# Performance work log

Measured on AMD Instinct MI355X. Metric: run time of the kernel, lower is better.

Reference implementation:

```python
import jax, jax.numpy as jnp
import numpy as np

HIDDEN = 2048
HEADS = 16
HEAD_DIM = HIDDEN // HEADS
BATCH = 2
SEQ = 2048


def setup_inputs() -> dict:
    key = jax.random.key(0)
    ks = jax.random.split(key, 9)
    s = 0.02
    return {
        "x": jax.random.normal(ks[0], (BATCH, SEQ, HIDDEN), dtype=jnp.float32),
        "wq": jax.random.normal(ks[1], (HIDDEN, HIDDEN), dtype=jnp.float32) * s,
        "bq": jax.random.normal(ks[2], (HIDDEN,), dtype=jnp.float32) * s,
        "wk": jax.random.normal(ks[3], (HIDDEN, HIDDEN), dtype=jnp.float32) * s,
        "bk": jax.random.normal(ks[4], (HIDDEN,), dtype=jnp.float32) * s,
        "wv": jax.random.normal(ks[5], (HIDDEN, HIDDEN), dtype=jnp.float32) * s,
        "bv": jax.random.normal(ks[6], (HIDDEN,), dtype=jnp.float32) * s,
        "wo": jax.random.normal(ks[7], (HIDDEN, HIDDEN), dtype=jnp.float32) * s,
        "bo": jax.random.normal(ks[8], (HIDDEN,), dtype=jnp.float32) * s,
    }


def reference(x, wq, bq, wk, bk, wv, bv, wo, bo):
    B, S, _ = x.shape
    scale = jnp.sqrt(jnp.float32(HEAD_DIM))
    # torch Linear: y = x @ W.T + b
    def proj(w, b):
        return (x @ w.T + b).reshape(B, S, HEADS, HEAD_DIM).transpose(0, 2, 1, 3)
    q = proj(wq, bq)  # [B,H,S,D]
    k = proj(wk, bk)
    v = proj(wv, bv)
    scores = jnp.einsum("bhqd,bhkd->bhqk", q, k) / scale  # [B,H,S,S]
    probs = jax.nn.softmax(scores, axis=-1)
    ctx = jnp.einsum("bhqk,bhkd->bhqd", probs, v)  # [B,H,S,D]
    ctx = ctx.transpose(0, 2, 1, 3).reshape(B, S, HIDDEN)
    return ctx @ wo.T + bo
```

## Files before the change

kernel.cpp:

```cpp
#include <hip/hip_runtime.h>

typedef unsigned short u16;
typedef unsigned int   u32;
typedef float  f32x4   __attribute__((ext_vector_type(4)));
typedef __bf16 bf16x8  __attribute__((ext_vector_type(8)));
typedef u16    u16x8   __attribute__((ext_vector_type(8)));
typedef u16    u16x4   __attribute__((ext_vector_type(4)));
typedef u32    u32x2   __attribute__((ext_vector_type(2)));
typedef u32    u32x4   __attribute__((ext_vector_type(4)));

#define HIDDEN 2048
#define SEQ    2048
#define NHEADS 16
#define HD     128
#define BATCH  2
#define QSTR   4096

typedef const __attribute__((address_space(3))) u16* lptr;

__device__ __forceinline__ u16 f2bf(float f) {
  u32 u = __builtin_bit_cast(u32, f);
  u += 0x7FFFu + ((u >> 16) & 1u);
  return (u16)(u >> 16);
}
__device__ __forceinline__ u32 pk2(float a, float b) {
  __bf16 x = (__bf16)a, y = (__bf16)b;
  return (u32)__builtin_bit_cast(u16, x) | ((u32)__builtin_bit_cast(u16, y) << 16);
}
__device__ __forceinline__ bf16x8 ld_frag(const u16* p) {
  return __builtin_bit_cast(bf16x8, *(const u32x4*)p);
}
__device__ __forceinline__ void gload_lds16(const u16* g, u16* l) {
  __builtin_amdgcn_global_load_lds((const __attribute__((address_space(1))) u32*)g,
                                   (__attribute__((address_space(3))) u32*)l, 16, 0, 0);
}

#define DSR(dst, base, lit) \
  asm volatile("ds_read_b128 %0, %1 offset:" lit : "=v"(dst) : "v"(base))

__global__ __launch_bounds__(256) void cvt_kernel(const float* __restrict__ src,
                                                  u16* __restrict__ dst, int n4) {
  int stride = gridDim.x * blockDim.x;
  for (int i = blockIdx.x * blockDim.x + threadIdx.x; i < n4; i += stride) {
    f32x4 v = ((const f32x4*)src)[i];
    u16x4 o;
    o[0] = f2bf(v[0]); o[1] = f2bf(v[1]); o[2] = f2bf(v[2]); o[3] = f2bf(v[3]);
    *(u16x4*)(dst + (size_t)i * 4) = o;
  }
}

__global__ __launch_bounds__(256) void cvt4_kernel(
    const float* __restrict__ s0, const float* __restrict__ s1,
    const float* __restrict__ s2, const float* __restrict__ s3,
    u16* __restrict__ o0, u16* __restrict__ o1,
    u16* __restrict__ o2, u16* __restrict__ o3, int n4) {
  const float* src = (blockIdx.y == 0) ? s0 : (blockIdx.y == 1) ? s1 : (blockIdx.y == 2) ? s2 : s3;
  u16* dst = (blockIdx.y == 0) ? o0 : (blockIdx.y == 1) ? o1 : (blockIdx.y == 2) ? o2 : o3;
  int stride = gridDim.x * blockDim.x;
  for (int i = blockIdx.x * blockDim.x + threadIdx.x; i < n4; i += stride) {
    f32x4 v = ((const f32x4*)src)[i];
    u16x4 o;
    o[0] = f2bf(v[0]); o[1] = f2bf(v[1]); o[2] = f2bf(v[2]); o[3] = f2bf(v[3]);
    *(u16x4*)(dst + (size_t)i * 4) = o;
  }
}

__global__ __launch_bounds__(512, 2) void gemm_qkv(
    const u16* __restrict__ A, const u16* __restrict__ Bt,
    const float* __restrict__ bq, const float* __restrict__ bk,
    const float* __restrict__ bv,
    u16* __restrict__ qk, u16* __restrict__ vtb, float qscale)
{
  __shared__ __attribute__((aligned(16))) u16 As[2][16384];
  __shared__ __attribute__((aligned(16))) u16 Bs[2][12288];

  const int tid  = threadIdx.x;
  const int lane = tid & 63;
  const int wave = tid >> 6;
  const int l15  = lane & 15;
  const int g    = lane >> 4;
  const int wm   = wave >> 2;
  const int wn   = wave & 3;

  const int id  = blockIdx.x;
  const int xcd = id & 7;
  const int c   = id >> 3;
  const int tileN = (xcd * 4 + (c >> 4)) * 192;
  const int tileM = (c & 15) << 8;

  const int srow = tid >> 3;
  const int gch8 = ((tid & 7) ^ (srow & 7)) * 8;
  const u16* agp = A  + (size_t)(tileM + srow) * HIDDEN + gch8;
  const u16* bgp = Bt + (size_t)(tileN + srow) * HIDDEN + gch8;
  u16* asp = (u16*)&As[0][0] + tid * 8;
  u16* bsp = (u16*)&Bs[0][0] + tid * 8;

  auto stage = [&](int buf, int ko) {
    u16* ad = asp + buf * 16384;
    u16* bd = bsp + buf * 12288;
#pragma unroll
    for (int r = 0; r < 4; ++r)
      gload_lds16(agp + (size_t)r * 64 * HIDDEN + ko, ad + r * 4096);
#pragma unroll
    for (int r = 0; r < 3; ++r)
      gload_lds16(bgp + (size_t)r * 64 * HIDDEN + ko, bd + r * 4096);
  };

  const int sw = l15 & 7;
  const int c0 = (g ^ sw) * 8;
  const int c1 = ((g ^ sw) ^ 4) * 8;
  lptr aT = (lptr)&As[0][0] + (size_t)(wm * 128 + l15) * 64;
  lptr bT = (lptr)&Bs[0][0] + (size_t)(wn * 48 + l15) * 64;

  f32x4 acc[8][3] = {};
  bf16x8 Xa[8], Xb[3], Ya[8], Yb[3];

#define ISSUE_SET(Sa, Sb, ab, bb)      \
  DSR(Sa[0], ab, "0");                 \
  DSR(Sa[1], ab, "2048");              \
  DSR(Sa[2], ab, "4096");              \
  DSR(Sa[3], ab, "6144");              \
  DSR(Sa[4], ab, "8192");              \
  DSR(Sa[5], ab, "10240");             \
  DSR(Sa[6], ab, "12288");             \
  DSR(Sa[7], ab, "14336");             \
  DSR(Sb[0], bb, "0");                 \
  DSR(Sb[1], bb, "2048");              \
  DSR(Sb[2], bb, "4096");

#define MFMA24(Sa, Sb)                                                                    \
  _Pragma("unroll")                                                                       \
  for (int mf = 0; mf < 8; ++mf) {                                                        \
    _Pragma("unroll")                                                                     \
    for (int nf = 0; nf < 3; ++nf)                                                        \
      acc[mf][nf] = __builtin_amdgcn_mfma_f32_16x16x32_bf16(Sa[mf], Sb[nf], acc[mf][nf], 0, 0, 0); \
  }

  stage(0, 0);
  stage(1, 64);
  asm volatile("s_waitcnt vmcnt(7)" ::: "memory");
  __builtin_amdgcn_s_barrier();
  __builtin_amdgcn_sched_barrier(0);
  {
    lptr ab = aT + c0;
    lptr bb = bT + c0;
    ISSUE_SET(Xa, Xb, ab, bb)
  }

#pragma unroll 2
  for (int t = 0; t < 32; ++t) {
    const int cur = t & 1;
    lptr aC = aT + cur * 16384;
    lptr bC = bT + cur * 12288;
    {
      lptr ab = aC + c1;
      lptr bb = bC + c1;
      ISSUE_SET(Ya, Yb, ab, bb)
    }
    asm volatile("s_waitcnt lgkmcnt(11)" ::: "memory");
    __builtin_amdgcn_sched_barrier(0);
    __builtin_amdgcn_s_setprio(1);
    MFMA24(Xa, Xb)
    __builtin_amdgcn_s_setprio(0);
    asm volatile("s_waitcnt lgkmcnt(0)" ::: "memory");
    __builtin_amdgcn_sched_barrier(0);
    __builtin_amdgcn_s_setprio(1);
    MFMA24(Ya, Yb)
    __builtin_amdgcn_s_setprio(0);
    __builtin_amdgcn_s_barrier();
    __builtin_amdgcn_sched_barrier(0);
    if (t < 30) {
      stage(cur, (t + 2) * 64);
      asm volatile("s_waitcnt vmcnt(7)" ::: "memory");
    } else {
      asm volatile("s_waitcnt vmcnt(0)" ::: "memory");
    }
    __builtin_amdgcn_s_barrier();
    __builtin_amdgcn_sched_barrier(0);
    if (t < 31) {
      lptr ab = aT + (cur ^ 1) * 16384 + c0;
      lptr bb = bT + (cur ^ 1) * 12288 + c0;
      ISSUE_SET(Xa, Xb, ab, bb)
    }
  }

#pragma unroll
  for (int mi = 0; mi < 8; ++mi) {
#pragma unroll
    for (int ni = 0; ni < 3; ++ni) {
      const int gcb = tileN + wn * 48 + ni * 16;
      const int seg = gcb >> 11;
      const int gc  = gcb + l15;
      const float bvv = ((seg == 0) ? bq : (seg == 1) ? bk : bv)[gc & 2047];
      if (seg < 2) {
        const float scl = (seg == 0) ? qscale : 1.f;
#pragma unroll
        for (int j = 0; j < 4; ++j) {
          const int gr = tileM + wm * 128 + mi * 16 + g * 4 + j;
          qk[(size_t)gr * QSTR + gc] = f2bf((acc[mi][ni][j] + bvv) * scl);
        }
      } else {
        const int dglob = gc - 4096;
        const int hh = dglob >> 7, dd = dglob & 127;
        const int srow0 = tileM + wm * 128 + mi * 16 + g * 4;
        const int bb = srow0 >> 11, ss = srow0 & 2047;
        u16x4 o;
#pragma unroll
        for (int j = 0; j < 4; ++j) o[j] = f2bf(acc[mi][ni][j] + bvv);
        *(u16x4*)(vtb + ((size_t)((bb * NHEADS + hh) * HD + dd)) * SEQ + ss) = o;
      }
    }
  }
#undef ISSUE_SET
#undef MFMA24
}

__global__ __launch_bounds__(256, 2) void gemm_bt(
    const u16* __restrict__ A, const u16* __restrict__ Bt,
    const float* __restrict__ bias, float* __restrict__ Cout,
    int M, int N, int K)
{
  __shared__ __attribute__((aligned(16))) u16 As[128 * 32];
  __shared__ __attribute__((aligned(16))) u16 Bs[128 * 32];
  const int tid  = threadIdx.x;
  const int lane = tid & 63;
  const int wave = tid >> 6;

  const int nbx   = N >> 7;
  const int nby   = M >> 7;
  const int id    = blockIdx.x;
  const int xcd   = id & 7;
  const int c     = id >> 3;
  const int cpx   = nbx >> 3;
  const int tileN = (xcd * cpx + c / nby) << 7;
  const int tileM = (c % nby) << 7;

  const int g = lane >> 4, r = lane & 15;

  const int srow = lane >> 2;
  const int scol = (lane & 3) * 8;
  const u16* ag0 = A  + (size_t)(tileM + wave * 16 + srow) * K + scol;
  const u16* ag1 = ag0 + (size_t)64 * K;
  const u16* bg0 = Bt + (size_t)(tileN + wave * 16 + srow) * K + scol;
  const u16* bg1 = bg0 + (size_t)64 * K;
  u16* as0 = &As[wave * 512];
  u16* as1 = &As[(wave + 4) * 512];
  u16* bs0 = &Bs[wave * 512];
  u16* bs1 = &Bs[(wave + 4) * 512];

  const int wm = wave >> 1, wn = wave & 1;
  const u16* afp = &As[(wm * 64 + r) * 32 + g * 8];
  const u16* bfp = &Bs[(wn * 64 + r) * 32 + g * 8];

  f32x4 acc[4][4] = {};

  for (int kt = 0; kt < K; kt += 32) {
    __syncthreads();
    gload_lds16(ag0 + kt, as0);
    gload_lds16(ag1 + kt, as1);
    gload_lds16(bg0 + kt, bs0);
    gload_lds16(bg1 + kt, bs1);
    __syncthreads();
    bf16x8 af[4], bf[4];
#pragma unroll
    for (int mi = 0; mi < 4; mi++) af[mi] = ld_frag(afp + mi * 512);
#pragma unroll
    for (int ni = 0; ni < 4; ni++) bf[ni] = ld_frag(bfp + ni * 512);
#pragma unroll
    for (int mi = 0; mi < 4; mi++)
#pragma unroll
      for (int ni = 0; ni < 4; ni++)
        acc[mi][ni] = __builtin_amdgcn_mfma_f32_16x16x32_bf16(af[mi], bf[ni], acc[mi][ni], 0, 0, 0);
  }

#pragma unroll
  for (int mi = 0; mi < 4; mi++) {
#pragma unroll
    for (int ni = 0; ni < 4; ni++) {
      const int gc = tileN + wn * 64 + ni * 16 + r;
      const float bv = bias[gc];
#pragma unroll
      for (int j = 0; j < 4; j++) {
        const int gr = tileM + wm * 64 + mi * 16 + g * 4 + j;
        Cout[(size_t)gr * N + gc] = acc[mi][ni][j] + bv;
      }
    }
  }
}

__global__ __launch_bounds__(256, 2) void attn_kernel(
    const u16* __restrict__ QKg, const u16* __restrict__ Vtg, u16* __restrict__ Ctx)
{
  __shared__ __attribute__((aligned(16))) u16 Ks[2][32 * 128];
  __shared__ __attribute__((aligned(16))) u16 Vs[2][128 * 32];

  const int tid  = threadIdx.x;
  const int lane = tid & 63;
  const int wave = tid >> 6;
  const int g4   = lane >> 4;
  const int l15  = lane & 15;

  const int wg = ((blockIdx.x & 7) << 6) + (blockIdx.x >> 3);
  const int bh = wg >> 4;
  const int qt = wg & 15;
  const int b  = bh >> 4, h = bh & 15;

  const u16* Qb  = QKg + (size_t)b * SEQ * QSTR + (size_t)h * HD;
  const u16* Kb  = Qb + 2048;
  const u16* Vth = Vtg + (size_t)bh * HD * SEQ;
  u16* Cb = Ctx + (size_t)b * SEQ * HIDDEN + (size_t)h * HD;

  const int qbase = qt * 128 + wave * 32 + l15;

  bf16x8 qf[2][4];
#pragma unroll
  for (int qs = 0; qs < 2; qs++)
#pragma unroll
    for (int dc = 0; dc < 4; dc++)
      qf[qs][dc] = ld_frag(Qb + (size_t)(qbase + qs * 16) * QSTR + dc * 32 + g4 * 8);

  const int kvp0 = (l15 >> 2) * 8 + (l15 & 3);
  const int msw  = (l15 & 3) | (((l15 >> 2) & 1) << 2);

  f32x4 ctx[2][8] = {};
  float m_run[2] = {-1e30f, -1e30f};
  float l_run[2] = {0.f, 0.f};

  auto stage = [&](int buf, int kv0) {
#pragma unroll
    for (int i = 0; i < 2; i++) {
      const int idx = tid + i * 256;
      const int kv = idx >> 4, up = idx & 15;
      const int um = up ^ ((kv & 3) | (((kv >> 3) & 1) << 2));
      gload_lds16(Kb + (size_t)(kv0 + kv) * QSTR + um * 8, &Ks[buf][idx * 8]);
      const int d = idx >> 2, u = idx & 3;
      gload_lds16(Vth + (size_t)d * SEQ + kv0 + u * 8, &Vs[buf][idx * 8]);
    }
  };

  stage(0, 0);
  __syncthreads();

  const int NT = SEQ / 32;
  for (int t = 0; t < NT; t++) {
    const int buf = t & 1;
    if (t + 1 < NT) stage(buf ^ 1, (t + 1) * 32);

    f32x4 s[2][2] = {};
    __builtin_amdgcn_s_setprio(1);
#pragma unroll
    for (int ni = 0; ni < 2; ni++) {
      const int row = kvp0 + ni * 4;
#pragma unroll
      for (int dc = 0; dc < 4; dc++) {
        bf16x8 kf = ld_frag(&Ks[buf][row * 128 + (((dc * 4 + g4) ^ msw) * 8)]);
        s[0][ni] = __builtin_amdgcn_mfma_f32_16x16x32_bf16(kf, qf[0][dc], s[0][ni], 0, 0, 0);
        s[1][ni] = __builtin_amdgcn_mfma_f32_16x16x32_bf16(kf, qf[1][dc], s[1][ni], 0, 0, 0);
      }
    }
    __builtin_amdgcn_s_setprio(0);

    bool ok0, ok1;
    float pmax[2];
#pragma unroll
    for (int qs = 0; qs < 2; qs++) {
      pmax[qs] = fmaxf(fmaxf(fmaxf(s[qs][0][0], s[qs][0][1]), fmaxf(s[qs][0][2], s[qs][0][3])),
                       fmaxf(fmaxf(s[qs][1][0], s[qs][1][1]), fmaxf(s[qs][1][2], s[qs][1][3])));
      pmax[qs] = fmaxf(pmax[qs], __shfl_xor(pmax[qs], 16));
      pmax[qs] = fmaxf(pmax[qs], __shfl_xor(pmax[qs], 32));
    }
    ok0 = (pmax[0] <= m_run[0] + 8.f);
    ok1 = (pmax[1] <= m_run[1] + 8.f);
    if (!__all(ok0 && ok1)) {
#pragma unroll
      for (int qs = 0; qs < 2; qs++) {
        const float mn = fmaxf(m_run[qs], pmax[qs]);
        const float corr = exp2f(m_run[qs] - mn);
        m_run[qs] = mn;
        l_run[qs] *= corr;
#pragma unroll
        for (int dt = 0; dt < 8; dt++)
#pragma unroll
          for (int j = 0; j < 4; j++) ctx[qs][dt][j] *= corr;
      }
    }
    bf16x8 pfrag[2];
#pragma unroll
    for (int qs = 0; qs < 2; qs++) {
      float ps = 0.f;
#pragma unroll
      for (int ni = 0; ni < 2; ni++)
#pragma unroll
        for (int j = 0; j < 4; j++) {
          const float p = exp2f(s[qs][ni][j] - m_run[qs]);
          s[qs][ni][j] = p;
          ps += p;
        }
      ps += __shfl_xor(ps, 16);
      ps += __shfl_xor(ps, 32);
      l_run[qs] += ps;
      u32x4 pw;
      pw[0] = pk2(s[qs][0][0], s[qs][0][1]);
      pw[1] = pk2(s[qs][0][2], s[qs][0][3]);
      pw[2] = pk2(s[qs][1][0], s[qs][1][1]);
      pw[3] = pk2(s[qs][1][2], s[qs][1][3]);
      pfrag[qs] = __builtin_bit_cast(bf16x8, pw);
    }

    __builtin_amdgcn_s_setprio(1);
#pragma unroll
    for (int dt = 0; dt < 8; dt++) {
      bf16x8 vf = ld_frag(&Vs[buf][(dt * 16 + l15) * 32 + g4 * 8]);
      ctx[0][dt] = __builtin_amdgcn_mfma_f32_16x16x32_bf16(vf, pfrag[0], ctx[0][dt], 0, 0, 0);
      ctx[1][dt] = __builtin_amdgcn_mfma_f32_16x16x32_bf16(vf, pfrag[1], ctx[1][dt], 0, 0, 0);
    }
    __builtin_amdgcn_s_setprio(0);

    __syncthreads();
  }

#pragma unroll
  for (int qs = 0; qs < 2; qs++) {
    const float linv = 1.f / l_run[qs];
    u16* crow = Cb + (size_t)(qbase + qs * 16) * HIDDEN;
#pragma unroll
    for (int dt = 0; dt < 8; dt++) {
      u16x4 o;
#pragma unroll
      for (int j = 0; j < 4; j++) o[j] = f2bf(ctx[qs][dt][j] * linv);
      *(u16x4*)&crow[dt * 16 + g4 * 4] = o;
    }
  }
}

extern "C" void kernel_launch(void* const* d_in, const int* in_sizes, int n_in,
                              void* d_out, int out_size, void* d_ws, size_t ws_size,
                              hipStream_t stream) {
  (void)in_sizes; (void)n_in; (void)out_size; (void)ws_size;
  const float* x  = (const float*)d_in[0];
  const float* wq = (const float*)d_in[1];
  const float* bq = (const float*)d_in[2];
  const float* wk = (const float*)d_in[3];
  const float* bk = (const float*)d_in[4];
  const float* wv = (const float*)d_in[5];
  const float* bv = (const float*)d_in[6];
  const float* wo = (const float*)d_in[7];
  const float* bo = (const float*)d_in[8];

  const size_t NX = (size_t)BATCH * SEQ * HIDDEN;
  const size_t NW = (size_t)HIDDEN * HIDDEN;
  u16* xb   = (u16*)d_ws;
  u16* wqb  = xb  + NX;
  u16* wkb  = wqb + NW;
  u16* wvb  = wkb + NW;
  u16* wob  = wvb + NW;
  u16* qk   = wob + NW;
  u16* vtb  = qk  + 2 * NX;
  u16* ctxb = xb;

  cvt_kernel<<<2048, 256, 0, stream>>>(x, xb, (int)(NX / 4));
  cvt4_kernel<<<dim3(512, 4), 256, 0, stream>>>(wq, wk, wv, wo, wqb, wkb, wvb, wob, (int)(NW / 4));

  const float qscale = 0.12751744174240807f;
  gemm_qkv<<<512, 512, 0, stream>>>(xb, wqb, bq, bk, bv, qk, vtb, qscale);

  attn_kernel<<<512, 256, 0, stream>>>(qk, vtb, ctxb);

  gemm_bt<<<512, 256, 0, stream>>>(ctxb, wob, bo, (float*)d_out, BATCH * SEQ, HIDDEN, HIDDEN);
}
```

Before: 289.6 us.

## Halve attention query tile per wave and double grid with V LDS swizzle

Each wave now handles 16 query rows instead of 32, so a workgroup covers 64 queries, the grid doubles to 1024 blocks and launch bounds allow 4 blocks per CU. This frees registers and raises occupancy so more waves can hide latency on the 256 CUs. In exchange every K/V tile is loaded and staged twice as often per query, because each staged tile now feeds half as many queries. An XOR swizzle is also added to the V staging and reads to cut LDS bank conflicts.

```diff
diff --git a/kernel.cpp b/kernel.cpp
--- a/kernel.cpp
+++ b/kernel.cpp
@@ -288,7 +288,7 @@
   }
 }
 
-__global__ __launch_bounds__(256, 2) void attn_kernel(
+__global__ __launch_bounds__(256, 4) void attn_kernel(
     const u16* __restrict__ QKg, const u16* __restrict__ Vtg, u16* __restrict__ Ctx)
 {
   __shared__ __attribute__((aligned(16))) u16 Ks[2][32 * 128];
@@ -300,9 +300,9 @@
   const int g4   = lane >> 4;
   const int l15  = lane & 15;
 
-  const int wg = ((blockIdx.x & 7) << 6) + (blockIdx.x >> 3);
-  const int bh = wg >> 4;
-  const int qt = wg & 15;
+  const int wg = ((blockIdx.x & 7) << 7) + (blockIdx.x >> 3);
+  const int bh = wg >> 5;
+  const int qt = wg & 31;
   const int b  = bh >> 4, h = bh & 15;
 
   const u16* Qb  = QKg + (size_t)b * SEQ * QSTR + (size_t)h * HD;
@@ -310,21 +310,20 @@
   const u16* Vth = Vtg + (size_t)bh * HD * SEQ;
   u16* Cb = Ctx + (size_t)b * SEQ * HIDDEN + (size_t)h * HD;
 
-  const int qbase = qt * 128 + wave * 32 + l15;
-
-  bf16x8 qf[2][4];
-#pragma unroll
-  for (int qs = 0; qs < 2; qs++)
-#pragma unroll
-    for (int dc = 0; dc < 4; dc++)
-      qf[qs][dc] = ld_frag(Qb + (size_t)(qbase + qs * 16) * QSTR + dc * 32 + g4 * 8);
+  const int qbase = qt * 64 + wave * 16 + l15;
+
+  bf16x8 qf[4];
+#pragma unroll
+  for (int dc = 0; dc < 4; dc++)
+    qf[dc] = ld_frag(Qb + (size_t)qbase * QSTR + dc * 32 + g4 * 8);
 
   const int kvp0 = (l15 >> 2) * 8 + (l15 & 3);
   const int msw  = (l15 & 3) | (((l15 >> 2) & 1) << 2);
-
-  f32x4 ctx[2][8] = {};
-  float m_run[2] = {-1e30f, -1e30f};
-  float l_run[2] = {0.f, 0.f};
+  const int vch  = (g4 ^ (l15 >> 2)) * 8;
+
+  f32x4 ctx[8] = {};
+  float m_run = -1e30f;
+  float l_run = 0.f;
 
   auto stage = [&](int buf, int kv0) {
 #pragma unroll
@@ -334,7 +333,8 @@
       const int um = up ^ ((kv & 3) | (((kv >> 3) & 1) << 2));
       gload_lds16(Kb + (size_t)(kv0 + kv) * QSTR + um * 8, &Ks[buf][idx * 8]);
       const int d = idx >> 2, u = idx & 3;
-      gload_lds16(Vth + (size_t)d * SEQ + kv0 + u * 8, &Vs[buf][idx * 8]);
+      const int uv = u ^ ((d >> 2) & 3);
+      gload_lds16(Vth + (size_t)d * SEQ + kv0 + uv * 8, &Vs[buf][idx * 8]);
     }
   };
 
@@ -346,7 +346,7 @@
     const int buf = t & 1;
     if (t + 1 < NT) stage(buf ^ 1, (t + 1) * 32);
 
-    f32x4 s[2][2] = {};
+    f32x4 s[2] = {};
     __builtin_amdgcn_s_setprio(1);
 #pragma unroll
     for (int ni = 0; ni < 2; ni++) {
@@ -354,82 +354,63 @@
 #pragma unroll
       for (int dc = 0; dc < 4; dc++) {
         bf16x8 kf = ld_frag(&Ks[buf][row * 128 + (((dc * 4 + g4) ^ msw) * 8)]);
-        s[0][ni] = __builtin_amdgcn_mfma_f32_16x16x32_bf16(kf, qf[0][dc], s[0][ni], 0, 0, 0);
-        s[1][ni] = __builtin_amdgcn_mfma_f32_16x16x32_bf16(kf, qf[1][dc], s[1][ni], 0, 0, 0);
+        s[ni] = __builtin_amdgcn_mfma_f32_16x16x32_bf16(kf, qf[dc], s[ni], 0, 0, 0);
       }
     }
     __builtin_amdgcn_s_setprio(0);
 
-    bool ok0, ok1;
-    float pmax[2];
-#pragma unroll
-    for (int qs = 0; qs < 2; qs++) {
-      pmax[qs] = fmaxf(fmaxf(fmaxf(s[qs][0][0], s[qs][0][1]), fmaxf(s[qs][0][2], s[qs][0][3])),
-                       fmaxf(fmaxf(s[qs][1][0], s[qs][1][1]), fmaxf(s[qs][1][2], s[qs][1][3])));
-      pmax[qs] = fmaxf(pmax[qs], __shfl_xor(pmax[qs], 16));
-      pmax[qs] = fmaxf(pmax[qs], __shfl_xor(pmax[qs], 32));
-    }
-    ok0 = (pmax[0] <= m_run[0] + 8.f);
-    ok1 = (pmax[1] <= m_run[1] + 8.f);
-    if (!__all(ok0 && ok1)) {
-#pragma unroll
-      for (int qs = 0; qs < 2; qs++) {
-        const float mn = fmaxf(m_run[qs], pmax[qs]);
-        const float corr = exp2f(m_run[qs] - mn);
-        m_run[qs] = mn;
-        l_run[qs] *= corr;
-#pragma unroll
-        for (int dt = 0; dt < 8; dt++)
-#pragma unroll
-          for (int j = 0; j < 4; j++) ctx[qs][dt][j] *= corr;
+    float pmax = fmaxf(fmaxf(fmaxf(s[0][0], s[0][1]), fmaxf(s[0][2], s[0][3])),
+                       fmaxf(fmaxf(s[1][0], s[1][1]), fmaxf(s[1][2], s[1][3])));
+    pmax = fmaxf(pmax, __shfl_xor(pmax, 16));
+    pmax = fmaxf(pmax, __shfl_xor(pmax, 32));
+    if (!__all(pmax <= m_run + 8.f)) {
+      const float mn = fmaxf(m_run, pmax);
+      const float corr = exp2f(m_run - mn);
+      m_run = mn;
+      l_run *= corr;
+#pragma unroll
+      for (int dt = 0; dt < 8; dt++)
+#pragma unroll
+        for (int j = 0; j < 4; j++) ctx[dt][j] *= corr;
+    }
+    float ps = 0.f;
+#pragma unroll
+    for (int ni = 0; ni < 2; ni++)
+#pragma unroll
+      for (int j = 0; j < 4; j++) {
+        const float p = exp2f(s[ni][j] - m_run);
+        s[ni][j] = p;
+        ps += p;
       }
-    }
-    bf16x8 pfrag[2];
-#pragma unroll
-    for (int qs = 0; qs < 2; qs++) {
-      float ps = 0.f;
-#pragma unroll
-      for (int ni = 0; ni < 2; ni++)
-#pragma unroll
-        for (int j = 0; j < 4; j++) {
-          const float p = exp2f(s[qs][ni][j] - m_run[qs]);
-          s[qs][ni][j] = p;
-          ps += p;
-        }
-      ps += __shfl_xor(ps, 16);
-      ps += __shfl_xor(ps, 32);
-      l_run[qs] += ps;
-      u32x4 pw;
-      pw[0] = pk2(s[qs][0][0], s[qs][0][1]);
-      pw[1] = pk2(s[qs][0][2], s[qs][0][3]);
-      pw[2] = pk2(s[qs][1][0], s[qs][1][1]);
-      pw[3] = pk2(s[qs][1][2], s[qs][1][3]);
-      pfrag[qs] = __builtin_bit_cast(bf16x8, pw);
-    }
+    ps += __shfl_xor(ps, 16);
+    ps += __shfl_xor(ps, 32);
+    l_run += ps;
+    u32x4 pw;
+    pw[0] = pk2(s[0][0], s[0][1]);
+    pw[1] = pk2(s[0][2], s[0][3]);
+    pw[2] = pk2(s[1][0], s[1][1]);
+    pw[3] = pk2(s[1][2], s[1][3]);
+    const bf16x8 pfrag = __builtin_bit_cast(bf16x8, pw);
 
     __builtin_amdgcn_s_setprio(1);
 #pragma unroll
     for (int dt = 0; dt < 8; dt++) {
-      bf16x8 vf = ld_frag(&Vs[buf][(dt * 16 + l15) * 32 + g4 * 8]);
-      ctx[0][dt] = __builtin_amdgcn_mfma_f32_16x16x32_bf16(vf, pfrag[0], ctx[0][dt], 0, 0, 0);
-      ctx[1][dt] = __builtin_amdgcn_mfma_f32_16x16x32_bf16(vf, pfrag[1], ctx[1][dt], 0, 0, 0);
+      bf16x8 vf = ld_frag(&Vs[buf][(dt * 16 + l15) * 32 + vch]);
+      ctx[dt] = __builtin_amdgcn_mfma_f32_16x16x32_bf16(vf, pfrag, ctx[dt], 0, 0, 0);
     }
     __builtin_amdgcn_s_setprio(0);
 
     __syncthreads();
   }
 
-#pragma unroll
-  for (int qs = 0; qs < 2; qs++) {
-    const float linv = 1.f / l_run[qs];
-    u16* crow = Cb + (size_t)(qbase + qs * 16) * HIDDEN;
-#pragma unroll
-    for (int dt = 0; dt < 8; dt++) {
-      u16x4 o;
-#pragma unroll
-      for (int j = 0; j < 4; j++) o[j] = f2bf(ctx[qs][dt][j] * linv);
-      *(u16x4*)&crow[dt * 16 + g4 * 4] = o;
-    }
+  const float linv = 1.f / l_run;
+  u16* crow = Cb + (size_t)qbase * HIDDEN;
+#pragma unroll
+  for (int dt = 0; dt < 8; dt++) {
+    u16x4 o;
+#pragma unroll
+    for (int j = 0; j < 4; j++) o[j] = f2bf(ctx[dt][j] * linv);
+    *(u16x4*)&crow[dt * 16 + g4 * 4] = o;
   }
 }
 
@@ -464,7 +445,7 @@
   const float qscale = 0.12751744174240807f;
   gemm_qkv<<<512, 512, 0, stream>>>(xb, wqb, bq, bk, bv, qk, vtb, qscale);
 
-  attn_kernel<<<512, 256, 0, stream>>>(qk, vtb, ctxb);
+  attn_kernel<<<1024, 256, 0, stream>>>(qk, vtb, ctxb);
 
   gemm_bt<<<512, 256, 0, stream>>>(ctxb, wob, bo, (float*)d_out, BATCH * SEQ, HIDDEN, HIDDEN);
 }
```

New measurement: 289.6 us. About the same (-0.0%).

## Widen attention KV tile to 64 with batched LDS reads and explicit waitcnt pipelining

Applied to the files above, without the earlier changes.

The attention kernel now processes 64 keys per iteration instead of 32, doubling the K/V LDS buffers. V gets an XOR-swizzled layout, and staging addresses are precomputed once outside the loop. K and V fragments are fetched up front with inline ds_read_b128, and MFMAs are split around partial lgkmcnt waits under sched_barriers. The full __syncthreads is replaced by explicit vmcnt waits plus s_barrier. The aim is to halve loop and barrier overhead and overlap LDS latency with MFMA work, at the cost of more LDS and registers, which may reduce occupancy.

```diff
diff --git a/kernel.cpp b/kernel.cpp
--- a/kernel.cpp
+++ b/kernel.cpp
@@ -37,6 +37,8 @@
 
 #define DSR(dst, base, lit) \
   asm volatile("ds_read_b128 %0, %1 offset:" lit : "=v"(dst) : "v"(base))
+
+#define MFMA16(d, a, b) d = __builtin_amdgcn_mfma_f32_16x16x32_bf16(a, b, d, 0, 0, 0)
 
 __global__ __launch_bounds__(256) void cvt_kernel(const float* __restrict__ src,
                                                   u16* __restrict__ dst, int n4) {
@@ -291,8 +293,8 @@
 __global__ __launch_bounds__(256, 2) void attn_kernel(
     const u16* __restrict__ QKg, const u16* __restrict__ Vtg, u16* __restrict__ Ctx)
 {
-  __shared__ __attribute__((aligned(16))) u16 Ks[2][32 * 128];
-  __shared__ __attribute__((aligned(16))) u16 Vs[2][128 * 32];
+  __shared__ __attribute__((aligned(16))) u16 Ks[2][64 * 128];
+  __shared__ __attribute__((aligned(16))) u16 Vs[2][128 * 64];
 
   const int tid  = threadIdx.x;
   const int lane = tid & 63;
@@ -321,56 +323,114 @@
 
   const int kvp0 = (l15 >> 2) * 8 + (l15 & 3);
   const int msw  = (l15 & 3) | (((l15 >> 2) & 1) << 2);
+  const int msw3 = msw & 3;
+  const int mk   = (l15 >> 2) & 1;
+  const int kcol = (g4 ^ msw3) * 8;
+
+  lptr ksb = (lptr)&Ks[0][0];
+  lptr kE0 = ksb + (kvp0      ) * 128 + kcol + mk * 32;
+  lptr kO0 = ksb + (kvp0      ) * 128 + kcol + (1 ^ mk) * 32;
+  lptr kE1 = ksb + (kvp0 +   4) * 128 + kcol + mk * 32;
+  lptr kO1 = ksb + (kvp0 +   4) * 128 + kcol + (1 ^ mk) * 32;
+  lptr kE2 = ksb + (kvp0 +  32) * 128 + kcol + mk * 32;
+  lptr kO2 = ksb + (kvp0 +  32) * 128 + kcol + (1 ^ mk) * 32;
+  lptr kE3 = ksb + (kvp0 +  36) * 128 + kcol + mk * 32;
+  lptr kO3 = ksb + (kvp0 +  36) * 128 + kcol + (1 ^ mk) * 32;
+
+  lptr vsb = (lptr)&Vs[0][0];
+  lptr vB0 = vsb + l15 * 64 + ((0 * 4 + g4) ^ (l15 & 7)) * 8;
+  lptr vB1 = vsb + l15 * 64 + ((1 * 4 + g4) ^ (l15 & 7)) * 8;
+
+  const u16* kg[4];
+  const u16* vg[4];
+  u16* ksd = (u16*)&Ks[0][0] + tid * 8;
+  u16* vsd = (u16*)&Vs[0][0] + tid * 8;
+#pragma unroll
+  for (int i = 0; i < 4; i++) {
+    const int idx = tid + i * 256;
+    const int kv = idx >> 4, up = idx & 15;
+    const int um = up ^ ((kv & 3) | (((kv >> 3) & 1) << 2));
+    kg[i] = Kb + (size_t)kv * QSTR + um * 8;
+    const int d = idx >> 3, u = idx & 7;
+    const int uv = u ^ (d & 7);
+    vg[i] = Vth + (size_t)d * SEQ + uv * 8;
+  }
+
+  auto stage = [&](int buf, int kv0) {
+    u16* kd = ksd + buf * 8192;
+    u16* vd = vsd + buf * 8192;
+#pragma unroll
+    for (int i = 0; i < 4; i++) gload_lds16(kg[i] + (size_t)kv0 * QSTR, kd + i * 2048);
+#pragma unroll
+    for (int i = 0; i < 4; i++) gload_lds16(vg[i] + kv0, vd + i * 2048);
+  };
 
   f32x4 ctx[2][8] = {};
   float m_run[2] = {-1e30f, -1e30f};
   float l_run[2] = {0.f, 0.f};
 
-  auto stage = [&](int buf, int kv0) {
-#pragma unroll
-    for (int i = 0; i < 2; i++) {
-      const int idx = tid + i * 256;
-      const int kv = idx >> 4, up = idx & 15;
-      const int um = up ^ ((kv & 3) | (((kv >> 3) & 1) << 2));
-      gload_lds16(Kb + (size_t)(kv0 + kv) * QSTR + um * 8, &Ks[buf][idx * 8]);
-      const int d = idx >> 2, u = idx & 3;
-      gload_lds16(Vth + (size_t)d * SEQ + kv0 + u * 8, &Vs[buf][idx * 8]);
-    }
-  };
-
   stage(0, 0);
-  __syncthreads();
-
-  const int NT = SEQ / 32;
+
+  const int NT = SEQ / 64;
   for (int t = 0; t < NT; t++) {
     const int buf = t & 1;
-    if (t + 1 < NT) stage(buf ^ 1, (t + 1) * 32);
-
-    f32x4 s[2][2] = {};
+
+    if (t + 1 < NT) {
+      stage(buf ^ 1, (t + 1) * 64);
+      asm volatile("s_waitcnt vmcnt(8)" ::: "memory");
+    } else {
+      asm volatile("s_waitcnt vmcnt(0)" ::: "memory");
+    }
+    __builtin_amdgcn_s_barrier();
+    __builtin_amdgcn_sched_barrier(0);
+
+    bf16x8 kf[4][4];
+    {
+      const int bo = buf * 8192;
+      lptr e0 = kE0 + bo, o0 = kO0 + bo, e1 = kE1 + bo, o1 = kO1 + bo;
+      lptr e2 = kE2 + bo, o2 = kO2 + bo, e3 = kE3 + bo, o3 = kO3 + bo;
+      DSR(kf[0][0], e0, "0"); DSR(kf[0][1], o0, "0"); DSR(kf[0][2], e0, "128"); DSR(kf[0][3], o0, "128");
+      DSR(kf[1][0], e1, "0"); DSR(kf[1][1], o1, "0"); DSR(kf[1][2], e1, "128"); DSR(kf[1][3], o1, "128");
+      DSR(kf[2][0], e2, "0"); DSR(kf[2][1], o2, "0"); DSR(kf[2][2], e2, "128"); DSR(kf[2][3], o2, "128");
+      DSR(kf[3][0], e3, "0"); DSR(kf[3][1], o3, "0"); DSR(kf[3][2], e3, "128"); DSR(kf[3][3], o3, "128");
+    }
+    f32x4 s[2][4] = {};
+    asm volatile("s_waitcnt lgkmcnt(8)" ::: "memory");
+    __builtin_amdgcn_sched_barrier(0);
     __builtin_amdgcn_s_setprio(1);
 #pragma unroll
-    for (int ni = 0; ni < 2; ni++) {
-      const int row = kvp0 + ni * 4;
+    for (int ni = 0; ni < 2; ni++)
 #pragma unroll
       for (int dc = 0; dc < 4; dc++) {
-        bf16x8 kf = ld_frag(&Ks[buf][row * 128 + (((dc * 4 + g4) ^ msw) * 8)]);
-        s[0][ni] = __builtin_amdgcn_mfma_f32_16x16x32_bf16(kf, qf[0][dc], s[0][ni], 0, 0, 0);
-        s[1][ni] = __builtin_amdgcn_mfma_f32_16x16x32_bf16(kf, qf[1][dc], s[1][ni], 0, 0, 0);
+        MFMA16(s[0][ni], kf[ni][dc], qf[0][dc]);
+        MFMA16(s[1][ni], kf[ni][dc], qf[1][dc]);
       }
-    }
+    __builtin_amdgcn_sched_barrier(0);
+    asm volatile("s_waitcnt lgkmcnt(0)" ::: "memory");
+    __builtin_amdgcn_sched_barrier(0);
+#pragma unroll
+    for (int ni = 2; ni < 4; ni++)
+#pragma unroll
+      for (int dc = 0; dc < 4; dc++) {
+        MFMA16(s[0][ni], kf[ni][dc], qf[0][dc]);
+        MFMA16(s[1][ni], kf[ni][dc], qf[1][dc]);
+      }
     __builtin_amdgcn_s_setprio(0);
-
-    bool ok0, ok1;
+    __builtin_amdgcn_sched_barrier(0);
+
     float pmax[2];
 #pragma unroll
     for (int qs = 0; qs < 2; qs++) {
-      pmax[qs] = fmaxf(fmaxf(fmaxf(s[qs][0][0], s[qs][0][1]), fmaxf(s[qs][0][2], s[qs][0][3])),
-                       fmaxf(fmaxf(s[qs][1][0], s[qs][1][1]), fmaxf(s[qs][1][2], s[qs][1][3])));
+      float m0 = fmaxf(fmaxf(s[qs][0][0], s[qs][0][1]), fmaxf(s[qs][0][2], s[qs][0][3]));
+      float m1 = fmaxf(fmaxf(s[qs][1][0], s[qs][1][1]), fmaxf(s[qs][1][2], s[qs][1][3]));
+      float m2 = fmaxf(fmaxf(s[qs][2][0], s[qs][2][1]), fmaxf(s[qs][2][2], s[qs][2][3]));
+      float m3 = fmaxf(fmaxf(s[qs][3][0], s[qs][3][1]), fmaxf(s[qs][3][2], s[qs][3][3]));
+      pmax[qs] = fmaxf(fmaxf(m0, m1), fmaxf(m2, m3));
       pmax[qs] = fmaxf(pmax[qs], __shfl_xor(pmax[qs], 16));
       pmax[qs] = fmaxf(pmax[qs], __shfl_xor(pmax[qs], 32));
     }
-    ok0 = (pmax[0] <= m_run[0] + 8.f);
-    ok1 = (pmax[1] <= m_run[1] + 8.f);
+    const bool ok0 = (pmax[0] <= m_run[0] + 8.f);
+    const bool ok1 = (pmax[1] <= m_run[1] + 8.f);
     if (!__all(ok0 && ok1)) {
 #pragma unroll
       for (int qs = 0; qs < 2; qs++) {
@@ -384,12 +444,12 @@
           for (int j = 0; j < 4; j++) ctx[qs][dt][j] *= corr;
       }
     }
-    bf16x8 pfrag[2];
+    bf16x8 pfrag[2][2];
 #pragma unroll
     for (int qs = 0; qs < 2; qs++) {
       float ps = 0.f;
 #pragma unroll
-      for (int ni = 0; ni < 2; ni++)
+      for (int ni = 0; ni < 4; ni++)
 #pragma unroll
         for (int j = 0; j < 4; j++) {
           const float p = exp2f(s[qs][ni][j] - m_run[qs]);
@@ -399,24 +459,52 @@
       ps += __shfl_xor(ps, 16);
       ps += __shfl_xor(ps, 32);
       l_run[qs] += ps;
-      u32x4 pw;
-      pw[0] = pk2(s[qs][0][0], s[qs][0][1]);
-      pw[1] = pk2(s[qs][0][2], s[qs][0][3]);
-      pw[2] = pk2(s[qs][1][0], s[qs][1][1]);
-      pw[3] = pk2(s[qs][1][2], s[qs][1][3]);
-      pfrag[qs] = __builtin_bit_cast(bf16x8, pw);
-    }
-
+#pragma unroll
+      for (int hh = 0; hh < 2; hh++) {
+        u32x4 pw;
+        pw[0] = pk2(s[qs][2 * hh][0], s[qs][2 * hh][1]);
+        pw[1] = pk2(s[qs][2 * hh][2], s[qs][2 * hh][3]);
+        pw[2] = pk2(s[qs][2 * hh + 1][0], s[qs][2 * hh + 1][1]);
+        pw[3] = pk2(s[qs][2 * hh + 1][2], s[qs][2 * hh + 1][3]);
+        pfrag[qs][hh] = __builtin_bit_cast(bf16x8, pw);
+      }
+    }
+    __builtin_amdgcn_sched_barrier(0);
+
+    bf16x8 vf[2][8];
+    {
+      lptr v0 = vB0 + buf * 8192;
+      lptr v1 = vB1 + buf * 8192;
+      DSR(vf[0][0], v0, "0");     DSR(vf[0][1], v0, "2048");
+      DSR(vf[0][2], v0, "4096");  DSR(vf[0][3], v0, "6144");
+      DSR(vf[0][4], v0, "8192");  DSR(vf[0][5], v0, "10240");
+      DSR(vf[0][6], v0, "12288"); DSR(vf[0][7], v0, "14336");
+      DSR(vf[1][0], v1, "0");     DSR(vf[1][1], v1, "2048");
+      DSR(vf[1][2], v1, "4096");  DSR(vf[1][3], v1, "6144");
+      DSR(vf[1][4], v1, "8192");  DSR(vf[1][5], v1, "10240");
+      DSR(vf[1][6], v1, "12288"); DSR(vf[1][7], v1, "14336");
+    }
+    asm volatile("s_waitcnt lgkmcnt(8)" ::: "memory");
+    __builtin_amdgcn_sched_barrier(0);
     __builtin_amdgcn_s_setprio(1);
 #pragma unroll
     for (int dt = 0; dt < 8; dt++) {
-      bf16x8 vf = ld_frag(&Vs[buf][(dt * 16 + l15) * 32 + g4 * 8]);
-      ctx[0][dt] = __builtin_amdgcn_mfma_f32_16x16x32_bf16(vf, pfrag[0], ctx[0][dt], 0, 0, 0);
-      ctx[1][dt] = __builtin_amdgcn_mfma_f32_16x16x32_bf16(vf, pfrag[1], ctx[1][dt], 0, 0, 0);
+      MFMA16(ctx[0][dt], vf[0][dt], pfrag[0][0]);
+      MFMA16(ctx[1][dt], vf[0][dt], pfrag[1][0]);
+    }
+    __builtin_amdgcn_sched_barrier(0);
+    asm volatile("s_waitcnt lgkmcnt(0)" ::: "memory");
+    __builtin_amdgcn_sched_barrier(0);
+#pragma unroll
+    for (int dt = 0; dt < 8; dt++) {
+      MFMA16(ctx[0][dt], vf[1][dt], pfrag[0][1]);
+      MFMA16(ctx[1][dt], vf[1][dt], pfrag[1][1]);
     }
     __builtin_amdgcn_s_setprio(0);
-
-    __syncthreads();
+    __builtin_amdgcn_sched_barrier(0);
+
+    __builtin_amdgcn_s_barrier();
+    __builtin_amdgcn_sched_barrier(0);
   }
 
 #pragma unroll
```

New measurement: 277.8 us. -4.1%, faster.
